# Optimization experiments

Measured on AMD Instinct MI355X. Metric: run time of the kernel, lower is better.

Reference implementation:

```python
import jax, jax.numpy as jnp
import numpy as np

N_WORD = 32000
N_CLASS = 5
N_HIDDEN = 32
T, B = 2048, 512

def setup_inputs() -> dict:
    key = jax.random.key(0)
    k_x, k_emb, k_w, k_b, k_cw, k_cb = jax.random.split(key, 6)
    x = jax.random.randint(k_x, (T, B), 0, N_WORD, dtype=jnp.int64 if jax.config.read('jax_enable_x64') else jnp.int32)
    s_emb = 1.0  # nn.Embedding default N(0,1)
    emb = jax.random.normal(k_emb, (N_WORD, N_HIDDEN), dtype=jnp.float32) * s_emb
    # nn.Linear default init: U(-1/sqrt(fan_in), 1/sqrt(fan_in))
    lim_rnn = 1.0 / np.sqrt(2 * N_HIDDEN)
    W_rnn = jax.random.uniform(k_w, (2 * N_HIDDEN, N_HIDDEN), jnp.float32, -lim_rnn, lim_rnn)
    b_rnn = jax.random.uniform(k_b, (N_HIDDEN,), jnp.float32, -lim_rnn, lim_rnn)
    lim_cls = 1.0 / np.sqrt(N_HIDDEN)
    W_cls = jax.random.uniform(k_cw, (N_HIDDEN, N_CLASS), jnp.float32, -lim_cls, lim_cls)
    b_cls = jax.random.uniform(k_cb, (N_CLASS,), jnp.float32, -lim_cls, lim_cls)
    return {"x": x, "emb": emb, "W_rnn": W_rnn, "b_rnn": b_rnn, "W_cls": W_cls, "b_cls": b_cls}

def reference(x, emb, W_rnn, b_rnn, W_cls, b_cls):
    # x: [T, B] int token ids. Embed -> [T, B, H]
    xe = emb[x]
    # Split W_rnn into the part applied to x_t and the part applied to h
    # (cat([xt, h]) @ W == xt @ W[:H] + h @ W[H:]), avoids per-step concat.
    Wx, Wh = W_rnn[:N_HIDDEN], W_rnn[N_HIDDEN:]
    h0 = jnp.zeros((x.shape[1], N_HIDDEN), dtype=emb.dtype)

    def step(h, xt):
        h = jnp.tanh(xt @ Wx + h @ Wh + b_rnn)
        return h, None

    h_final, _ = jax.lax.scan(step, h0, xe)
    y = h_final @ W_cls + b_cls  # [B, n_class]
    return y
```

## Files before the change

### kernel.cpp

```cpp
#include <hip/hip_runtime.h>
#include <hip/hip_bf16.h>

#define TT 2048
#define BB 512
#define HH 32
#define NPAIR (TT * BB)
#define PSTRIDE (BB * HH)

#define PIN(x) asm volatile("" : "+v"(x))

__device__ __forceinline__ float fast_tanh(float u) {
    float e = exp2f(u * 2.88539008177792681f);
    return fmaf(__builtin_amdgcn_rcpf(e + 1.0f), -2.0f, 1.0f);
}

template <int N>
__device__ __forceinline__ float dpp_ror(float v) {
    return __int_as_float(__builtin_amdgcn_mov_dpp(
        __float_as_int(v), 0x120 | N, 0xF, 0xF, false));
}
__device__ __forceinline__ float swz_x16(float v) {
    return __int_as_float(__builtin_amdgcn_ds_swizzle(__float_as_int(v), 0x401F));
}

__global__ __launch_bounds__(256) void precompute_v11(
        const int* __restrict__ x, const float* __restrict__ emb,
        const float* __restrict__ W_rnn, const float* __restrict__ b_rnn,
        __hip_bfloat16* __restrict__ P) {
    const int tid = threadIdx.x;
    const int jj  = tid & 31;
    const int l   = tid & 63;
    const int grp = tid >> 5;
    const int g   = (blockIdx.x * 256 + tid) >> 5;
    const int pair0 = g * 16;

    __shared__ float stage[8][16][HH];

    float wx[32];
#pragma unroll
    for (int k = 0; k < 32; ++k) wx[k] = W_rnn[k * HH + jj];
    const float bj = b_rnn[jj];

    const int idxv  = x[pair0 + (jj & 15)];
    const int bbase = (l & 32) * 4;

    float ev[16];
#pragma unroll
    for (int i = 0; i < 16; ++i) {
        int pi = __builtin_amdgcn_ds_bpermute(bbase + 4 * i, idxv);
        ev[i] = emb[(size_t)pi * HH + jj];
    }
#pragma unroll
    for (int i = 0; i < 16; ++i)
        stage[grp][i][jj] = ev[i];

#pragma unroll 4
    for (int i = 0; i < 16; ++i) {
        const float4* sp = (const float4*)&stage[grp][i][0];
        float u0 = bj, u1 = 0.f, u2 = 0.f, u3 = 0.f;
#pragma unroll
        for (int q = 0; q < 8; ++q) {
            float4 e = sp[q];
            u0 = fmaf(e.x, wx[4*q+0], u0);
            u1 = fmaf(e.y, wx[4*q+1], u1);
            u2 = fmaf(e.z, wx[4*q+2], u2);
            u3 = fmaf(e.w, wx[4*q+3], u3);
        }
        P[(size_t)(pair0 + i) * HH + jj] = __float2bfloat16((u0 + u1) + (u2 + u3));
    }
}

__global__ __launch_bounds__(64, 1) void rnn_seq_v11(
        const __hip_bfloat16* __restrict__ P, const float* __restrict__ W_rnn,
        const float* __restrict__ W_cls, const float* __restrict__ b_cls,
        float* __restrict__ out) {
    const int l = threadIdx.x;
    const int i = l & 15;
    const int q = (l >> 4) & 1;

    int rt = __builtin_amdgcn_mov_dpp(i, 0x121, 0xF, 0xF, false);
    const int d = (rt == ((i + 1) & 15)) ? 1 : -1;

    float wKeep[16], wSend[16];
#pragma unroll
    for (int o = 0; o < 16; ++o) {
        const int k = q * 16 + ((i + d * o) & 15);
        wKeep[o] = W_rnn[(HH + k) * HH + (q * 16 + i)];
        wSend[o] = W_rnn[(HH + k) * HH + ((q ^ 1) * 16 + i)];
    }
#pragma unroll
    for (int o = 0; o < 16; ++o) { PIN(wKeep[o]); PIN(wSend[o]); }

    const __hip_bfloat16* gp = P + (size_t)blockIdx.x * 64 + l;

    float pA[8], pB[8];
#pragma unroll
    for (int t = 0; t < 8; ++t)
        pA[t] = __bfloat162float(gp[(size_t)t * PSTRIDE]);

    float h = 0.0f;

    auto step = [&](float p) {
        float rot[16];
        rot[0] = h;
        rot[1] = dpp_ror<1>(h);
        rot[2] = dpp_ror<2>(h);
        rot[3] = dpp_ror<3>(h);
#pragma unroll
        for (int m = 1; m < 4; ++m) {
            rot[4*m+0] = dpp_ror<4>(rot[4*m-4]);
            rot[4*m+1] = dpp_ror<4>(rot[4*m-3]);
            rot[4*m+2] = dpp_ror<4>(rot[4*m-2]);
            rot[4*m+3] = dpp_ror<4>(rot[4*m-1]);
        }
        float s0 = rot[0] * wSend[0], s1 = rot[1] * wSend[1];
        float s2 = rot[2] * wSend[2], s3 = rot[3] * wSend[3];
#pragma unroll
        for (int m = 1; m < 4; ++m) {
            s0 = fmaf(rot[4*m+0], wSend[4*m+0], s0);
            s1 = fmaf(rot[4*m+1], wSend[4*m+1], s1);
            s2 = fmaf(rot[4*m+2], wSend[4*m+2], s2);
            s3 = fmaf(rot[4*m+3], wSend[4*m+3], s3);
        }
        float send = (s0 + s1) + (s2 + s3);
        float recv = swz_x16(send);
        float k0 = fmaf(rot[0], wKeep[0], p), k1 = rot[1] * wKeep[1];
        float k2 = rot[2] * wKeep[2],         k3 = rot[3] * wKeep[3];
#pragma unroll
        for (int m = 1; m < 4; ++m) {
            k0 = fmaf(rot[4*m+0], wKeep[4*m+0], k0);
            k1 = fmaf(rot[4*m+1], wKeep[4*m+1], k1);
            k2 = fmaf(rot[4*m+2], wKeep[4*m+2], k2);
            k3 = fmaf(rot[4*m+3], wKeep[4*m+3], k3);
        }
        float u = ((k0 + k1) + (k2 + k3)) + recv;
        h = fast_tanh(u);
    };

#pragma unroll 1
    for (int e = 0; e < TT / 16; ++e) {
        const int tB = e * 16 + 8;
#pragma unroll
        for (int t = 0; t < 8; ++t)
            pB[t] = __bfloat162float(gp[(size_t)(tB + t) * PSTRIDE]);
#pragma unroll
        for (int t = 0; t < 8; ++t) PIN(pA[t]);
#pragma unroll
        for (int s = 0; s < 8; ++s) step(pA[s]);

        int tA = e * 16 + 16;
        if (tA > TT - 8) tA = TT - 8;
#pragma unroll
        for (int t = 0; t < 8; ++t)
            pA[t] = __bfloat162float(gp[(size_t)(tA + t) * PSTRIDE]);
#pragma unroll
        for (int t = 0; t < 8; ++t) PIN(pB[t]);
#pragma unroll
        for (int s = 0; s < 8; ++s) step(pB[s]);
    }

    __shared__ float hf[64];
    hf[l] = h;
    if (l < 10) {
        const int rr = l / 5, c = l % 5;
        float acc = b_cls[c];
#pragma unroll
        for (int k = 0; k < 32; ++k)
            acc = fmaf(hf[rr * 32 + k], W_cls[k * 5 + c], acc);
        out[(blockIdx.x * 2 + rr) * 5 + c] = acc;
    }
}

__device__ __forceinline__ float rnn_step_fb(const float4 xt[8], const float wx[32],
                                             const float wh[32], float bj,
                                             float* hrow, int lane) {
    float u0 = 0.f, u1 = 0.f, u2 = 0.f, u3 = 0.f;
#pragma unroll
    for (int q = 0; q < 8; ++q) {
        u0 = fmaf(xt[q].x, wx[4*q+0], u0);
        u1 = fmaf(xt[q].y, wx[4*q+1], u1);
        u2 = fmaf(xt[q].z, wx[4*q+2], u2);
        u3 = fmaf(xt[q].w, wx[4*q+3], u3);
    }
    const float4* hp = (const float4*)hrow;
#pragma unroll
    for (int q = 0; q < 8; ++q) {
        float4 hv = hp[q];
        u0 = fmaf(hv.x, wh[4*q+0], u0);
        u1 = fmaf(hv.y, wh[4*q+1], u1);
        u2 = fmaf(hv.z, wh[4*q+2], u2);
        u3 = fmaf(hv.w, wh[4*q+3], u3);
    }
    float hn = fast_tanh(bj + ((u0 + u1) + (u2 + u3)));
    hrow[lane] = hn;
    return hn;
}

__global__ __launch_bounds__(64, 1) void rnn_seq_kernel(
        const int* __restrict__ x, const float* __restrict__ emb,
        const float* __restrict__ W_rnn, const float* __restrict__ b_rnn,
        const float* __restrict__ W_cls, const float* __restrict__ b_cls,
        float* __restrict__ out) {
    const int lane = threadIdx.x & 31;
    const int grp  = threadIdx.x >> 5;
    const int row  = blockIdx.x * 2 + grp;
    __shared__ float hbuf[2][HH];
    float wx[32], wh[32];
#pragma unroll
    for (int k = 0; k < 32; ++k) {
        wx[k] = W_rnn[k * HH + lane];
        wh[k] = W_rnn[(HH + k) * HH + lane];
    }
    const float bj = b_rnn[lane];
    hbuf[grp][lane] = 0.0f;
    float* hrow = &hbuf[grp][0];
    int i1 = x[1 * BB + row];
    float4 xcur[8], xnxt[8];
    {
        int i0 = x[0 * BB + row];
        const float4* ep = (const float4*)(emb + (size_t)i0 * HH);
#pragma unroll
        for (int q = 0; q < 8; ++q) xcur[q] = ep[q];
    }
    for (int t = 0; t < TT; t += 2) {
        int i2 = x[min(t + 2, TT - 1) * BB + row];
        {
            const float4* ep = (const float4*)(emb + (size_t)i1 * HH);
#pragma unroll
            for (int q = 0; q < 8; ++q) xnxt[q] = ep[q];
        }
        rnn_step_fb(xcur, wx, wh, bj, hrow, lane);
        i1 = x[min(t + 3, TT - 1) * BB + row];
        {
            const float4* ep = (const float4*)(emb + (size_t)i2 * HH);
#pragma unroll
            for (int q = 0; q < 8; ++q) xcur[q] = ep[q];
        }
        rnn_step_fb(xnxt, wx, wh, bj, hrow, lane);
    }
    if (lane < 5) {
        float acc = b_cls[lane];
#pragma unroll
        for (int k = 0; k < 32; ++k)
            acc = fmaf(hrow[k], W_cls[k * 5 + lane], acc);
        out[row * 5 + lane] = acc;
    }
}

extern "C" void kernel_launch(void* const* d_in, const int* in_sizes, int n_in,
                              void* d_out, int out_size, void* d_ws, size_t ws_size,
                              hipStream_t stream) {
    const int*   x     = (const int*)d_in[0];
    const float* emb   = (const float*)d_in[1];
    const float* W_rnn = (const float*)d_in[2];
    const float* b_rnn = (const float*)d_in[3];
    const float* W_cls = (const float*)d_in[4];
    const float* b_cls = (const float*)d_in[5];
    float* out = (float*)d_out;

    const size_t need16 = (size_t)NPAIR * HH * 2;
    if (ws_size >= need16) {
        __hip_bfloat16* P = (__hip_bfloat16*)d_ws;
        const int pre_blocks = NPAIR / (16 * 8);
        precompute_v11<<<pre_blocks, 256, 0, stream>>>(x, emb, W_rnn, b_rnn, P);
        rnn_seq_v11<<<BB / 2, 64, 0, stream>>>(P, W_rnn, W_cls, b_cls, out);
    } else {
        rnn_seq_kernel<<<BB / 2, 64, 0, stream>>>(x, emb, W_rnn, b_rnn, W_cls, b_cls, out);
    }
}
```

Before: 399.4 us.

## Compute input projection with bf16 MFMA and fold tanh scale into weights

The embedding-gather input projection is replaced with a kernel where each wave gathers 16 embedding rows and computes the 16x32 projection with two bf16 MFMA 16x16x32 instructions. This removes the LDS staging and scalar FMA loops. The 2/ln2 tanh exponent scale is pre-multiplied into the precomputed projection, the bias and the recurrent weights, so the sequential step drops one multiply from its critical path. Inputs and input weights are now rounded to bf16 before the product, which adds rounding error.

```diff
diff --git a/kernel.cpp b/kernel.cpp
--- a/kernel.cpp
+++ b/kernel.cpp
@@ -6,11 +6,16 @@
 #define HH 32
 #define NPAIR (TT * BB)
 #define PSTRIDE (BB * HH)
+#define CSC 2.88539008177792681f
 
 #define PIN(x) asm volatile("" : "+v"(x))
 
+__device__ __forceinline__ float fast_tanh_pre(float u) {
+    float e = exp2f(u);
+    return fmaf(__builtin_amdgcn_rcpf(e + 1.0f), -2.0f, 1.0f);
+}
 __device__ __forceinline__ float fast_tanh(float u) {
-    float e = exp2f(u * 2.88539008177792681f);
+    float e = exp2f(u * CSC);
     return fmaf(__builtin_amdgcn_rcpf(e + 1.0f), -2.0f, 1.0f);
 }
 
@@ -23,54 +28,53 @@
     return __int_as_float(__builtin_amdgcn_ds_swizzle(__float_as_int(v), 0x401F));
 }
 
-__global__ __launch_bounds__(256) void precompute_v11(
+__device__ __forceinline__ short f2bf(float f) {
+    __hip_bfloat16 h = __float2bfloat16(f);
+    return *reinterpret_cast<short*>(&h);
+}
+
+typedef __attribute__((ext_vector_type(8))) short bf16x8;
+typedef __attribute__((ext_vector_type(4))) float f32x4;
+
+__global__ __launch_bounds__(256) void precompute_mfma(
         const int* __restrict__ x, const float* __restrict__ emb,
         const float* __restrict__ W_rnn, const float* __restrict__ b_rnn,
         __hip_bfloat16* __restrict__ P) {
-    const int tid = threadIdx.x;
-    const int jj  = tid & 31;
-    const int l   = tid & 63;
-    const int grp = tid >> 5;
-    const int g   = (blockIdx.x * 256 + tid) >> 5;
-    const int pair0 = g * 16;
-
-    __shared__ float stage[8][16][HH];
-
-    float wx[32];
-#pragma unroll
-    for (int k = 0; k < 32; ++k) wx[k] = W_rnn[k * HH + jj];
-    const float bj = b_rnn[jj];
-
-    const int idxv  = x[pair0 + (jj & 15)];
-    const int bbase = (l & 32) * 4;
-
-    float ev[16];
-#pragma unroll
-    for (int i = 0; i < 16; ++i) {
-        int pi = __builtin_amdgcn_ds_bpermute(bbase + 4 * i, idxv);
-        ev[i] = emb[(size_t)pi * HH + jj];
-    }
-#pragma unroll
-    for (int i = 0; i < 16; ++i)
-        stage[grp][i][jj] = ev[i];
-
-#pragma unroll 4
-    for (int i = 0; i < 16; ++i) {
-        const float4* sp = (const float4*)&stage[grp][i][0];
-        float u0 = bj, u1 = 0.f, u2 = 0.f, u3 = 0.f;
-#pragma unroll
-        for (int q = 0; q < 8; ++q) {
-            float4 e = sp[q];
-            u0 = fmaf(e.x, wx[4*q+0], u0);
-            u1 = fmaf(e.y, wx[4*q+1], u1);
-            u2 = fmaf(e.z, wx[4*q+2], u2);
-            u3 = fmaf(e.w, wx[4*q+3], u3);
-        }
-        P[(size_t)(pair0 + i) * HH + jj] = __float2bfloat16((u0 + u1) + (u2 + u3));
-    }
-}
-
-__global__ __launch_bounds__(64, 1) void rnn_seq_v11(
+    const int l  = threadIdx.x & 63;
+    const int wv = (blockIdx.x * 256 + threadIdx.x) >> 6;
+    const int pair0 = wv * 16;
+    const int m  = l & 15;
+    const int kb = (l >> 4) * 8;
+
+    bf16x8 bf0, bf1;
+#pragma unroll
+    for (int j = 0; j < 8; ++j) {
+        bf0[j] = f2bf(CSC * W_rnn[(kb + j) * HH + m]);
+        bf1[j] = f2bf(CSC * W_rnn[(kb + j) * HH + m + 16]);
+    }
+
+    const int idx = x[pair0 + m];
+    const float4* ep = (const float4*)(emb + (size_t)idx * HH + kb);
+    float4 e0 = ep[0], e1 = ep[1];
+    bf16x8 af;
+    af[0] = f2bf(e0.x); af[1] = f2bf(e0.y); af[2] = f2bf(e0.z); af[3] = f2bf(e0.w);
+    af[4] = f2bf(e1.x); af[5] = f2bf(e1.y); af[6] = f2bf(e1.z); af[7] = f2bf(e1.w);
+
+    const float bn0 = CSC * b_rnn[m], bn1 = CSC * b_rnn[m + 16];
+    f32x4 c0 = {bn0, bn0, bn0, bn0};
+    f32x4 c1 = {bn1, bn1, bn1, bn1};
+    c0 = __builtin_amdgcn_mfma_f32_16x16x32_bf16(af, bf0, c0, 0, 0, 0);
+    c1 = __builtin_amdgcn_mfma_f32_16x16x32_bf16(af, bf1, c1, 0, 0, 0);
+
+#pragma unroll
+    for (int reg = 0; reg < 4; ++reg) {
+        const int row = (l >> 4) * 4 + reg;
+        P[(size_t)(pair0 + row) * HH + m]      = __float2bfloat16(c0[reg]);
+        P[(size_t)(pair0 + row) * HH + m + 16] = __float2bfloat16(c1[reg]);
+    }
+}
+
+__global__ __launch_bounds__(64, 1) void rnn_seq_v13(
         const __hip_bfloat16* __restrict__ P, const float* __restrict__ W_rnn,
         const float* __restrict__ W_cls, const float* __restrict__ b_cls,
         float* __restrict__ out) {
@@ -85,8 +89,8 @@
 #pragma unroll
     for (int o = 0; o < 16; ++o) {
         const int k = q * 16 + ((i + d * o) & 15);
-        wKeep[o] = W_rnn[(HH + k) * HH + (q * 16 + i)];
-        wSend[o] = W_rnn[(HH + k) * HH + ((q ^ 1) * 16 + i)];
+        wKeep[o] = CSC * W_rnn[(HH + k) * HH + (q * 16 + i)];
+        wSend[o] = CSC * W_rnn[(HH + k) * HH + ((q ^ 1) * 16 + i)];
     }
 #pragma unroll
     for (int o = 0; o < 16; ++o) { PIN(wKeep[o]); PIN(wSend[o]); }
@@ -134,7 +138,7 @@
             k3 = fmaf(rot[4*m+3], wKeep[4*m+3], k3);
         }
         float u = ((k0 + k1) + (k2 + k3)) + recv;
-        h = fast_tanh(u);
+        h = fast_tanh_pre(u);
     };
 
 #pragma unroll 1
@@ -261,9 +265,9 @@
     const size_t need16 = (size_t)NPAIR * HH * 2;
     if (ws_size >= need16) {
         __hip_bfloat16* P = (__hip_bfloat16*)d_ws;
-        const int pre_blocks = NPAIR / (16 * 8);
-        precompute_v11<<<pre_blocks, 256, 0, stream>>>(x, emb, W_rnn, b_rnn, P);
-        rnn_seq_v11<<<BB / 2, 64, 0, stream>>>(P, W_rnn, W_cls, b_cls, out);
+        const int pre_blocks = NPAIR / (16 * 4);
+        precompute_mfma<<<pre_blocks, 256, 0, stream>>>(x, emb, W_rnn, b_rnn, P);
+        rnn_seq_v13<<<BB / 2, 64, 0, stream>>>(P, W_rnn, W_cls, b_cls, out);
     } else {
         rnn_seq_kernel<<<BB / 2, 64, 0, stream>>>(x, emb, W_rnn, b_rnn, W_cls, b_cls, out);
     }
```

Result: faster. 371.4 us (-7.0%).
